# Kernel tuning notes

Measured on AMD Instinct MI355X. Metric: run time of the kernel, lower is better.

The kernel has to match this reference:

```python
import jax, jax.numpy as jnp
import numpy as np

N_NODES = 50000
N_EDGES = 262144
N_OCP = 32768
N_GRAPHS = 64
H = 128          # hidden_size
F_IN = 128       # node feature dim (== H for the stub GNN)
N_LABELS = 10


def _lin(key, fan_in, fan_out):
    return jax.random.normal(key, (fan_in, fan_out), jnp.float32) * (1.0 / float(np.sqrt(fan_in)))


def setup_inputs() -> dict:
    key = jax.random.key(0)
    ks = jax.random.split(key, 16)
    x = jax.random.normal(ks[0], (N_NODES, F_IN), jnp.float32)
    edge_index = jax.random.randint(ks[1], (2, N_EDGES), 0, N_NODES)
    batch_vec = jnp.sort(jax.random.randint(ks[2], (N_NODES,), 0, N_GRAPHS))
    y = jax.random.randint(ks[3], (N_GRAPHS,), 0, N_LABELS)
    params = {
        # stub GNN (get_node_reps): one GCN-style layer
        'W_self': _lin(ks[4], F_IN, H),
        'W_nbr': _lin(ks[5], F_IN, H),
        'b_gnn': jnp.zeros((H,), jnp.float32),
        # edge_action_rep_generator: Linear(2H,4H) ELU Linear(4H,2H) ELU Linear(2H,H)
        'Wr1': _lin(ks[6], 2 * H, 4 * H), 'br1': jnp.zeros((4 * H,), jnp.float32),
        'Wr2': _lin(ks[7], 4 * H, 2 * H), 'br2': jnp.zeros((2 * H,), jnp.float32),
        'Wr3': _lin(ks[8], 2 * H, H),     'br3': jnp.zeros((H,), jnp.float32),
        # edge_action_prob_generator: Linear(H,H) ELU Linear(H,num_labels)
        'Wp1': _lin(ks[9], H, H),         'bp1': jnp.zeros((H,), jnp.float32),
        'Wp2': _lin(ks[10], H, N_LABELS), 'bp2': jnp.zeros((N_LABELS,), jnp.float32),
    }
    return dict(x=x, edge_index=edge_index, batch_vec=batch_vec, y=y, n_ocp=N_OCP, **params)


def reference(x, edge_index, batch_vec, y, n_ocp,
              W_self, W_nbr, b_gnn,
              Wr1, br1, Wr2, br2, Wr3, br3,
              Wp1, bp1, Wp2, bp2):
    N = x.shape[0]
    G = y.shape[0]

    def get_node_reps(ei):
        # stub for self.model.get_node_reps: elu(x @ W_self + A @ (x @ W_nbr))
        msg = x[ei[0]] @ W_nbr                                   # [E', H]
        agg = jax.ops.segment_sum(msg, ei[1], num_segments=N)    # [N, H]
        return jax.nn.elu(x @ W_self + agg + b_gnn)

    ocp_edge_index = edge_index[:, :n_ocp]    # state == True edges
    ava_edge_index = edge_index[:, n_ocp:]    # state == False edges

    ava_node_reps = get_node_reps(edge_index) - get_node_reps(ocp_edge_index)  # [N, H]

    # gather per available edge + concat src/dst reps -> [E_ava, 2H]
    a = jnp.concatenate([ava_node_reps[ava_edge_index[0]],
                         ava_node_reps[ava_edge_index[1]]], axis=1)
    # edge_action_rep_generator
    a = jax.nn.elu(a @ Wr1 + br1)
    a = jax.nn.elu(a @ Wr2 + br2)
    a = a @ Wr3 + br3                                            # [E_ava, H]
    # edge_action_prob_generator
    h = jax.nn.elu(a @ Wp1 + bp1)
    logits = h @ Wp2 + bp2                                       # [E_ava, L]

    seg = batch_vec[ava_edge_index[0]]                           # graph id per ava edge
    y_edge = y[seg]                                              # target label per edge
    sel = jnp.take_along_axis(logits, y_edge[:, None], axis=1)[:, 0]  # gather(1, y)

    # segment-wise softmax over edges of each graph
    mx = jax.ops.segment_max(sel, seg, num_segments=G)
    ex = jnp.exp(sel - mx[seg])
    probs = ex / jax.ops.segment_sum(ex, seg, num_segments=G)[seg]    # [E_ava]

    # scatter_max: per-graph max prob and its argmax edge index
    pmax = jax.ops.segment_max(probs, seg, num_segments=G)            # [G]
    E = probs.shape[0]
    idx = jnp.where(probs == pmax[seg], jnp.arange(E), E)
    added_actions = jax.ops.segment_min(idx, seg, num_segments=G)     # [G]

    return probs, pmax, added_actions
```

## Files before the change

### kernel.cpp

```cpp
#include <hip/hip_runtime.h>

#define NN   50000
#define NNP  50048
#define NE   262144
#define NOCP 32768
#define EAVA (NE - NOCP)
#define NG   64
#define HD   128
#define CAP  48
#define CHNK 32768

typedef _Float16 f16x8 __attribute__((ext_vector_type(8)));
typedef _Float16 f16x2 __attribute__((ext_vector_type(2)));
typedef float f32x4 __attribute__((ext_vector_type(4)));

__device__ __forceinline__ float elu_f(float v) { return v > 0.f ? v : (expf(v) - 1.f); }

__device__ __forceinline__ unsigned fenc(float f) {
  unsigned u = __float_as_uint(f);
  return (u & 0x80000000u) ? ~u : (u | 0x80000000u);
}
__device__ __forceinline__ float fdec(unsigned u) {
  return __uint_as_float((u & 0x80000000u) ? (u & 0x7fffffffu) : ~u);
}

__device__ __forceinline__ void dma16(const void* g, void* l) {
  __builtin_amdgcn_global_load_lds((const __attribute__((address_space(1))) unsigned int*)g,
                                   (__attribute__((address_space(3))) unsigned int*)l,
                                   16, 0, 0);
}

__global__ __launch_bounds__(256) void zero_i(int* __restrict__ p, int n) {
  for (int i = blockIdx.x * 256 + threadIdx.x; i < n; i += gridDim.x * 256) p[i] = 0;
}

__global__ void init_small(unsigned* mx_enc, float* denom, unsigned* pmax_enc, int* amin) {
  int t = threadIdx.x;
  if (t < NG) { mx_enc[t] = 0u; denom[t] = 0.f; pmax_enc[t] = 0u; amin[t] = EAVA; }
}

__global__ __launch_bounds__(256) void zero_tails(_Float16* __restrict__ base) {
  int t = blockIdx.x * 256 + threadIdx.x;
  if (t >= 6 * 768) return;
  int arr = t / 768, off = t % 768;
  f16x8 z = {};
  *(f16x8*)(base + (size_t)arr * NNP * HD + (size_t)NN * HD + (size_t)off * 8) = z;
}

__global__ __launch_bounds__(256) void bucket_kernel(const int* __restrict__ ei,
    int* __restrict__ cnt, int* __restrict__ bucket) {
  int e = blockIdx.x * 256 + threadIdx.x;
  if (e >= NE) return;
  int dst = ei[NE + e];
  int slot = atomicAdd(&cnt[dst], 1);
  if (slot < CAP) bucket[(size_t)dst * CAP + slot] = e;
}

__global__ __launch_bounds__(256) void gather_kernel(const float* __restrict__ x,
    const int* __restrict__ ei, const int* __restrict__ cnt, const int* __restrict__ bucket,
    _Float16* __restrict__ xsah, _Float16* __restrict__ xsal,
    _Float16* __restrict__ xsoh, _Float16* __restrict__ xsol) {
  int n = blockIdx.x * 4 + (threadIdx.x >> 6);
  if (n >= NN) return;
  int lane = threadIdx.x & 63;
  int c = cnt[n];
  if (c > CAP) c = CAP;
  float2 aall = make_float2(0.f, 0.f), aocp = aall;
  const int* bk = bucket + (size_t)n * CAP;
  for (int i = 0; i < c; ++i) {
    int e = bk[i];
    int src = ei[e];
    float2 v = *(const float2*)(x + (size_t)src * HD + lane * 2);
    aall.x += v.x; aall.y += v.y;
    if (e < NOCP) { aocp.x += v.x; aocp.y += v.y; }
  }
  size_t o = (size_t)n * HD + lane * 2;
  _Float16 h0 = (_Float16)aall.x, h1 = (_Float16)aall.y;
  *(f16x2*)(xsah + o) = (f16x2){h0, h1};
  *(f16x2*)(xsal + o) = (f16x2){(_Float16)(aall.x - (float)h0), (_Float16)(aall.y - (float)h1)};
  _Float16 g0 = (_Float16)aocp.x, g1 = (_Float16)aocp.y;
  *(f16x2*)(xsoh + o) = (f16x2){g0, g1};
  *(f16x2*)(xsol + o) = (f16x2){(_Float16)(aocp.x - (float)g0), (_Float16)(aocp.y - (float)g1)};
}

__global__ __launch_bounds__(256) void split_x(const float* __restrict__ r,
    _Float16* __restrict__ rh, _Float16* __restrict__ rl) {
  int t = blockIdx.x * 256 + threadIdx.x;
  if (t >= NN * HD / 8) return;
  const float4* p = (const float4*)(r + (size_t)t * 8);
  float4 v0 = p[0], v1 = p[1];
  float vv[8] = {v0.x, v0.y, v0.z, v0.w, v1.x, v1.y, v1.z, v1.w};
  f16x8 hv, lv;
#pragma unroll
  for (int j = 0; j < 8; ++j) {
    _Float16 hh = (_Float16)vv[j];
    hv[j] = hh;
    lv[j] = (_Float16)(vv[j] - (float)hh);
  }
  *(f16x8*)(rh + (size_t)t * 8) = hv;
  *(f16x8*)(rl + (size_t)t * 8) = lv;
}

__global__ void pack_w2(const float* __restrict__ Wself, const float* __restrict__ Wnbr,
    _Float16* __restrict__ oh, _Float16* __restrict__ ol) {
  int chunk = blockIdx.x;
  int lane = threadIdx.x;
  int ns = chunk & 7, kt = chunk >> 3;
  int n = ns * 16 + (lane & 15);
  int k0 = kt * 32 + (lane >> 4) * 8;
  f16x8 hv, lv;
#pragma unroll
  for (int j = 0; j < 8; ++j) {
    int k = k0 + j;
    float v = (k < 128) ? Wself[(size_t)k * 128 + n] : Wnbr[(size_t)(k - 128) * 128 + n];
    _Float16 hh = (_Float16)v;
    hv[j] = hh;
    lv[j] = (_Float16)(v - (float)hh);
  }
  *(f16x8*)(oh + (size_t)chunk * 512 + lane * 8) = hv;
  *(f16x8*)(ol + (size_t)chunk * 512 + lane * 8) = lv;
}

__global__ void pack_w(const float* __restrict__ W, int K, int N,
    _Float16* __restrict__ oh, _Float16* __restrict__ ol) {
  int chunk = blockIdx.x;
  int lane = threadIdx.x;
  int NS = N >> 4;
  int ns = chunk % NS, kt = chunk / NS;
  int n = ns * 16 + (lane & 15);
  int k0 = kt * 32 + (lane >> 4) * 8;
  f16x8 hv, lv;
#pragma unroll
  for (int j = 0; j < 8; ++j) {
    float v = W[(size_t)(k0 + j) * N + n];
    _Float16 hh = (_Float16)v;
    hv[j] = hh;
    lv[j] = (_Float16)(v - (float)hh);
  }
  *(f16x8*)(oh + (size_t)chunk * 512 + lane * 8) = hv;
  *(f16x8*)(ol + (size_t)chunk * 512 + lane * 8) = lv;
}

__global__ void w34_kernel(const float* __restrict__ Wr3, const float* __restrict__ Wp1,
    const float* __restrict__ br3, const float* __restrict__ bp1,
    float* __restrict__ W34, float* __restrict__ b34) {
  int i = blockIdx.x, j = threadIdx.x;
  float s = 0.f;
  for (int k = 0; k < 128; ++k) s += Wr3[i * 128 + k] * Wp1[k * 128 + j];
  W34[i * 128 + j] = s;
  if (i == 0) {
    float t = bp1[j];
    for (int k = 0; k < 128; ++k) t += br3[k] * Wp1[k * 128 + j];
    b34[j] = t;
  }
}

template <int KT, int NS_B, int AMODE, int KT_NEXT>
__global__ __launch_bounds__(256) void gemm_ab(
    const _Float16* __restrict__ Ah, const _Float16* __restrict__ Al,
    const int* __restrict__ idx0, const int* __restrict__ idx1,
    const _Float16* __restrict__ Bh, const _Float16* __restrict__ Bl,
    const float* __restrict__ bias,
    _Float16* __restrict__ Oh, _Float16* __restrict__ Ol) {
  __shared__ char smem[65536] __attribute__((aligned(16)));
  float* sC = (float*)smem;

  const int tid = threadIdx.x;
  const int w = tid >> 6, lane = tid & 63;
  const int l16 = lane & 15, g16 = lane >> 4;
  const int bm = blockIdx.x * 128, bn = blockIdx.y * 128;
  const int mw = (w >> 1) * 4, nw = (w & 1) * 4;
  const int bmT = bm >> 4, bnS = bn >> 4;

  f32x4 acc[4][4];
#pragma unroll
  for (int i = 0; i < 4; ++i)
#pragma unroll
    for (int j = 0; j < 4; ++j) acc[i][j] = (f32x4)0.f;

  int i0a = 0, i0b = 0, i1a = 0, i1b = 0;
  if constexpr (AMODE == 1) {
    int rr0 = bm + w * 32 + l16;
    i0a = idx0[rr0]; i0b = idx0[rr0 + 16];
    i1a = idx1[rr0]; i1b = idx1[rr0 + 16];
  }

  auto STAGE = [&](int kt, int buf) {
    char* base = smem + buf * 32768;
    if constexpr (AMODE == 0) {
#pragma unroll
      for (int s = 0; s < 2; ++s) {
        int msub = w * 2 + s;
        size_t ch = (size_t)(bmT + msub) * KT + kt;
        dma16((const char*)Ah + ch * 1024 + lane * 16, base + msub * 1024);
        dma16((const char*)Al + ch * 1024 + lane * 16, base + 8192 + msub * 1024);
      }
    } else {
      int col = (kt & 3) * 32 + g16 * 8;
      int r0 = (kt < 4) ? i0a : i1a;
      int r1 = (kt < 4) ? i0b : i1b;
      dma16(Ah + (size_t)r0 * HD + col, base + (w * 2) * 1024);
      dma16(Al + (size_t)r0 * HD + col, base + 8192 + (w * 2) * 1024);
      dma16(Ah + (size_t)r1 * HD + col, base + (w * 2 + 1) * 1024);
      dma16(Al + (size_t)r1 * HD + col, base + 8192 + (w * 2 + 1) * 1024);
    }
#pragma unroll
    for (int s = 0; s < 2; ++s) {
      int nsub = w * 2 + s;
      size_t ch = (size_t)kt * NS_B + bnS + nsub;
      dma16((const char*)Bh + ch * 1024 + lane * 16, base + 16384 + nsub * 1024);
      dma16((const char*)Bl + ch * 1024 + lane * 16, base + 24576 + nsub * 1024);
    }
  };

  auto COMPUTE = [&](int buf) {
    const _Float16* sAh = (const _Float16*)(smem + buf * 32768);
    const _Float16* sAl = (const _Float16*)(smem + buf * 32768 + 8192);
    const _Float16* sBh = (const _Float16*)(smem + buf * 32768 + 16384);
    const _Float16* sBl = (const _Float16*)(smem + buf * 32768 + 24576);
    f16x8 ah[4], al[4];
#pragma unroll
    for (int mi = 0; mi < 4; ++mi) {
      ah[mi] = *(const f16x8*)(sAh + (mw + mi) * 512 + lane * 8);
      al[mi] = *(const f16x8*)(sAl + (mw + mi) * 512 + lane * 8);
    }
#pragma unroll
    for (int ni = 0; ni < 4; ++ni) {
      f16x8 bh = *(const f16x8*)(sBh + (nw + ni) * 512 + lane * 8);
      f16x8 bl = *(const f16x8*)(sBl + (nw + ni) * 512 + lane * 8);
#pragma unroll
      for (int mi = 0; mi < 4; ++mi) {
        acc[mi][ni] = __builtin_amdgcn_mfma_f32_16x16x32_f16(ah[mi], bh, acc[mi][ni], 0, 0, 0);
        acc[mi][ni] = __builtin_amdgcn_mfma_f32_16x16x32_f16(al[mi], bh, acc[mi][ni], 0, 0, 0);
        acc[mi][ni] = __builtin_amdgcn_mfma_f32_16x16x32_f16(ah[mi], bl, acc[mi][ni], 0, 0, 0);
      }
    }
  };

  STAGE(0, 0);
  __builtin_amdgcn_s_waitcnt(0);
  __syncthreads();
  for (int kt = 0; kt < KT; kt += 2) {
    STAGE(kt + 1, 1);
    COMPUTE(0);
    __builtin_amdgcn_s_waitcnt(0);
    __syncthreads();
    if (kt + 2 < KT) STAGE(kt + 2, 0);
    COMPUTE(1);
    __builtin_amdgcn_s_waitcnt(0);
    __syncthreads();
  }

  const int bnT32 = bn >> 5;
  for (int ph = 0; ph < 2; ++ph) {
    if ((w & 1) == ph) {
#pragma unroll
      for (int ni = 0; ni < 4; ++ni) {
        int colL = ni * 16 + l16;
        float bv = bias[bn + ph * 64 + colL];
#pragma unroll
        for (int mi = 0; mi < 4; ++mi) {
          int rowb = (mw + mi) * 16 + g16 * 4;
#pragma unroll
          for (int r = 0; r < 4; ++r)
            sC[(rowb + r) * 68 + colL] = elu_f(acc[mi][ni][r] + bv);
        }
      }
    }
    __syncthreads();
#pragma unroll
    for (int c = 0; c < 4; ++c) {
      int chunkid = w * 4 + c;
      int msub = chunkid >> 1, ktl = chunkid & 1;
      int m = msub * 16 + l16;
      int cb = ktl * 32 + g16 * 8;
      f16x8 hv, lv;
#pragma unroll
      for (int j = 0; j < 8; ++j) {
        float v = sC[m * 68 + cb + j];
        _Float16 hh = (_Float16)v;
        hv[j] = hh;
        lv[j] = (_Float16)(v - (float)hh);
      }
      size_t gchunk = (size_t)(bmT + msub) * KT_NEXT + (bnT32 + ph * 2 + ktl);
      *(f16x8*)((char*)Oh + gchunk * 1024 + lane * 16) = hv;
      *(f16x8*)((char*)Ol + gchunk * 1024 + lane * 16) = lv;
    }
    __syncthreads();
  }
}

__global__ __launch_bounds__(64) void reps_direct(
    const _Float16* __restrict__ xh, const _Float16* __restrict__ xl,
    const _Float16* __restrict__ xsah, const _Float16* __restrict__ xsal,
    const _Float16* __restrict__ xsoh, const _Float16* __restrict__ xsol,
    const _Float16* __restrict__ Wsh, const _Float16* __restrict__ Wsl,
    const float* __restrict__ bias,
    _Float16* __restrict__ Oh, _Float16* __restrict__ Ol) {
  __shared__ float sC[64][68];
  const int lane = threadIdx.x;
  const int mt = blockIdx.x, nt = blockIdx.y;
  const int bm = mt * 64, bn = nt * 64;
  const int l16 = lane & 15, g16 = lane >> 4;

  f32x4 acc1[4][4], acc2[4][4];
#pragma unroll
  for (int i = 0; i < 4; ++i)
#pragma unroll
    for (int j = 0; j < 4; ++j) acc1[i][j] = (f32x4)0.f;

  auto CP3 = [&](f32x4 (*acc)[4], const f16x8* ah, const f16x8* al,
                 const f16x8* bh, const f16x8* bl) {
#pragma unroll
    for (int ni = 0; ni < 4; ++ni)
#pragma unroll
      for (int mi = 0; mi < 4; ++mi) {
        acc[mi][ni] = __builtin_amdgcn_mfma_f32_16x16x32_f16(ah[mi], bh[ni], acc[mi][ni], 0, 0, 0);
        acc[mi][ni] = __builtin_amdgcn_mfma_f32_16x16x32_f16(al[mi], bh[ni], acc[mi][ni], 0, 0, 0);
        acc[mi][ni] = __builtin_amdgcn_mfma_f32_16x16x32_f16(ah[mi], bl[ni], acc[mi][ni], 0, 0, 0);
      }
  };

#pragma unroll
  for (int kt = 0; kt < 4; ++kt) {
    f16x8 ah[4], al[4], bh[4], bl[4];
#pragma unroll
    for (int mi = 0; mi < 4; ++mi) {
      size_t off = (size_t)(bm + mi * 16 + l16) * HD + kt * 32 + g16 * 8;
      ah[mi] = *(const f16x8*)(xh + off);
      al[mi] = *(const f16x8*)(xl + off);
    }
#pragma unroll
    for (int ni = 0; ni < 4; ++ni) {
      size_t ch = (size_t)kt * 8 + nt * 4 + ni;
      bh[ni] = *(const f16x8*)(Wsh + ch * 512 + lane * 8);
      bl[ni] = *(const f16x8*)(Wsl + ch * 512 + lane * 8);
    }
    CP3(acc1, ah, al, bh, bl);
  }
#pragma unroll
  for (int i = 0; i < 4; ++i)
#pragma unroll
    for (int j = 0; j < 4; ++j) acc2[i][j] = acc1[i][j];

#pragma unroll
  for (int kt = 0; kt < 4; ++kt) {
    f16x8 aah[4], aal[4], aoh[4], aol[4], bh[4], bl[4];
#pragma unroll
    for (int mi = 0; mi < 4; ++mi) {
      size_t off = (size_t)(bm + mi * 16 + l16) * HD + kt * 32 + g16 * 8;
      aah[mi] = *(const f16x8*)(xsah + off);
      aal[mi] = *(const f16x8*)(xsal + off);
      aoh[mi] = *(const f16x8*)(xsoh + off);
      aol[mi] = *(const f16x8*)(xsol + off);
    }
#pragma unroll
    for (int ni = 0; ni < 4; ++ni) {
      size_t ch = (size_t)(kt + 4) * 8 + nt * 4 + ni;
      bh[ni] = *(const f16x8*)(Wsh + ch * 512 + lane * 8);
      bl[ni] = *(const f16x8*)(Wsl + ch * 512 + lane * 8);
    }
    CP3(acc1, aah, aal, bh, bl);
    CP3(acc2, aoh, aol, bh, bl);
  }

#pragma unroll
  for (int ni = 0; ni < 4; ++ni) {
    int colL = ni * 16 + l16;
    float bv = bias[bn + colL];
#pragma unroll
    for (int mi = 0; mi < 4; ++mi) {
      int rowb = mi * 16 + g16 * 4;
#pragma unroll
      for (int r = 0; r < 4; ++r)
        sC[rowb + r][colL] = elu_f(acc1[mi][ni][r] + bv) - elu_f(acc2[mi][ni][r] + bv);
    }
  }
  __syncthreads();
#pragma unroll
  for (int c = 0; c < 8; ++c) {
    int msub = c >> 1, ktl = c & 1;
    int m = msub * 16 + l16;
    int cb = ktl * 32 + g16 * 8;
    int grow = bm + m;
    if (grow < NN) {
      f16x8 hv, lv;
#pragma unroll
      for (int j = 0; j < 8; ++j) {
        float v = sC[m][cb + j];
        _Float16 hh = (_Float16)v;
        hv[j] = hh;
        lv[j] = (_Float16)(v - (float)hh);
      }
      *(f16x8*)(Oh + (size_t)grow * HD + bn + cb) = hv;
      *(f16x8*)(Ol + (size_t)grow * HD + bn + cb) = lv;
    }
  }
}

__global__ __launch_bounds__(256) void gemm3_sel(
    const _Float16* __restrict__ Ah, const _Float16* __restrict__ Al,
    const _Float16* __restrict__ Bh, const _Float16* __restrict__ Bl,
    const float* __restrict__ b34,
    const int* __restrict__ ei, const int* __restrict__ batchv, const int* __restrict__ yv,
    const float* __restrict__ Wp2, const float* __restrict__ bp2,
    float* __restrict__ sel, int* __restrict__ seg, int co) {
  __shared__ char smem[65536] __attribute__((aligned(16)));
  const int tid = threadIdx.x;
  const int w = tid >> 6, lane = tid & 63;
  const int l16 = lane & 15, g16 = lane >> 4;
  const int mt = blockIdx.x;

  f32x4 acc[2][8];
#pragma unroll
  for (int i = 0; i < 2; ++i)
#pragma unroll
    for (int j = 0; j < 8; ++j) acc[i][j] = (f32x4)0.f;

  auto STAGE = [&](int kt, int buf) {
    char* base = smem + buf * 32768;
#pragma unroll
    for (int s = 0; s < 2; ++s) {
      int msub = w * 2 + s;
      size_t ch = (size_t)(mt * 8 + msub) * 8 + kt;
      dma16((const char*)Ah + ch * 1024 + lane * 16, base + msub * 1024);
      dma16((const char*)Al + ch * 1024 + lane * 16, base + 8192 + msub * 1024);
    }
#pragma unroll
    for (int s = 0; s < 2; ++s) {
      int nsub = w * 2 + s;
      size_t ch = (size_t)kt * 8 + nsub;
      dma16((const char*)Bh + ch * 1024 + lane * 16, base + 16384 + nsub * 1024);
      dma16((const char*)Bl + ch * 1024 + lane * 16, base + 24576 + nsub * 1024);
    }
  };

  auto COMPUTE = [&](int buf) {
    const _Float16* sAh = (const _Float16*)(smem + buf * 32768);
    const _Float16* sAl = (const _Float16*)(smem + buf * 32768 + 8192);
    const _Float16* sBh = (const _Float16*)(smem + buf * 32768 + 16384);
    const _Float16* sBl = (const _Float16*)(smem + buf * 32768 + 24576);
    f16x8 ah[2], al[2];
#pragma unroll
    for (int mi = 0; mi < 2; ++mi) {
      ah[mi] = *(const f16x8*)(sAh + (w * 2 + mi) * 512 + lane * 8);
      al[mi] = *(const f16x8*)(sAl + (w * 2 + mi) * 512 + lane * 8);
    }
#pragma unroll
    for (int ni = 0; ni < 8; ++ni) {
      f16x8 bh = *(const f16x8*)(sBh + ni * 512 + lane * 8);
      f16x8 bl = *(const f16x8*)(sBl + ni * 512 + lane * 8);
#pragma unroll
      for (int mi = 0; mi < 2; ++mi) {
        acc[mi][ni] = __builtin_amdgcn_mfma_f32_16x16x32_f16(ah[mi], bh, acc[mi][ni], 0, 0, 0);
        acc[mi][ni] = __builtin_amdgcn_mfma_f32_16x16x32_f16(al[mi], bh, acc[mi][ni], 0, 0, 0);
        acc[mi][ni] = __builtin_amdgcn_mfma_f32_16x16x32_f16(ah[mi], bl, acc[mi][ni], 0, 0, 0);
      }
    }
  };

  STAGE(0, 0);
  __builtin_amdgcn_s_waitcnt(0);
  __syncthreads();
  for (int kt = 0; kt < 8; kt += 2) {
    STAGE(kt + 1, 1);
    COMPUTE(0);
    __builtin_amdgcn_s_waitcnt(0);
    __syncthreads();
    if (kt + 2 < 8) STAGE(kt + 2, 0);
    COMPUTE(1);
    __builtin_amdgcn_s_waitcnt(0);
    __syncthreads();
  }

  float bb[8];
#pragma unroll
  for (int ni = 0; ni < 8; ++ni) bb[ni] = b34[ni * 16 + l16];

#pragma unroll
  for (int mi = 0; mi < 2; ++mi)
#pragma unroll
    for (int rr = 0; rr < 4; ++rr) {
      int row = w * 32 + mi * 16 + g16 * 4 + rr;
      int e = co + mt * 128 + row;
      int s = ei[NOCP + e];
      int gg = batchv[s];
      int c = yv[gg];
      float a = 0.f;
#pragma unroll
      for (int ni = 0; ni < 8; ++ni)
        a += elu_f(acc[mi][ni][rr] + bb[ni]) * Wp2[(ni * 16 + l16) * 10 + c];
      a += __shfl_xor(a, 1);
      a += __shfl_xor(a, 2);
      a += __shfl_xor(a, 4);
      a += __shfl_xor(a, 8);
      if (l16 == 0) { sel[e] = a + bp2[c]; seg[e] = gg; }
    }
}

__global__ __launch_bounds__(256) void segmax_sel(const float* __restrict__ sel,
    const int* __restrict__ seg, unsigned* __restrict__ mx_enc) {
  __shared__ unsigned sm[NG];
  int tid = threadIdx.x;
  if (tid < NG) sm[tid] = 0u;
  __syncthreads();
  for (int i = blockIdx.x * blockDim.x + tid; i < EAVA; i += gridDim.x * blockDim.x)
    atomicMax(&sm[seg[i]], fenc(sel[i]));
  __syncthreads();
  if (tid < NG) atomicMax(&mx_enc[tid], sm[tid]);
}

__global__ __launch_bounds__(256) void exden_kernel(const float* __restrict__ sel,
    const int* __restrict__ seg, const unsigned* __restrict__ mx_enc,
    float* __restrict__ denom, float* __restrict__ out_probs) {
  __shared__ float sd[NG];
  __shared__ float smx[NG];
  int tid = threadIdx.x;
  if (tid < NG) { smx[tid] = fdec(mx_enc[tid]); sd[tid] = 0.f; }
  __syncthreads();
  for (int i = blockIdx.x * blockDim.x + tid; i < EAVA; i += gridDim.x * blockDim.x) {
    int g = seg[i];
    float ex = expf(sel[i] - smx[g]);
    out_probs[i] = ex;
    atomicAdd(&sd[g], ex);
  }
  __syncthreads();
  if (tid < NG) atomicAdd(&denom[tid], sd[tid]);
}

__global__ __launch_bounds__(256) void probpmax_kernel(const int* __restrict__ seg,
    const float* __restrict__ denom, float* __restrict__ out_probs,
    unsigned* __restrict__ pmax_enc) {
  __shared__ float sden[NG];
  __shared__ unsigned sp[NG];
  int tid = threadIdx.x;
  if (tid < NG) { sden[tid] = denom[tid]; sp[tid] = 0u; }
  __syncthreads();
  for (int i = blockIdx.x * blockDim.x + tid; i < EAVA; i += gridDim.x * blockDim.x) {
    int g = seg[i];
    float p = out_probs[i] / sden[g];
    out_probs[i] = p;
    atomicMax(&sp[g], fenc(p));
  }
  __syncthreads();
  if (tid < NG) atomicMax(&pmax_enc[tid], sp[tid]);
}

__global__ __launch_bounds__(256) void argmin_kernel(const int* __restrict__ seg,
    const float* __restrict__ out_probs, const unsigned* __restrict__ pmax_enc,
    int* __restrict__ amin) {
  __shared__ float spm[NG];
  __shared__ int sa[NG];
  int tid = threadIdx.x;
  if (tid < NG) { spm[tid] = fdec(pmax_enc[tid]); sa[tid] = EAVA; }
  __syncthreads();
  for (int i = blockIdx.x * blockDim.x + tid; i < EAVA; i += gridDim.x * blockDim.x) {
    int g = seg[i];
    if (out_probs[i] == spm[g]) atomicMin(&sa[g], i);
  }
  __syncthreads();
  if (tid < NG) atomicMin(&amin[tid], sa[tid]);
}

__global__ void finalize_kernel(const unsigned* __restrict__ pmax_enc,
    const int* __restrict__ amin, float* __restrict__ out) {
  int g = threadIdx.x;
  if (g < NG) {
    out[EAVA + g] = fdec(pmax_enc[g]);
    out[EAVA + NG + g] = (float)amin[g];
  }
}

extern "C" void kernel_launch(void* const* d_in, const int* in_sizes, int n_in,
                              void* d_out, int out_size, void* d_ws, size_t ws_size,
                              hipStream_t stream) {
  const float* x      = (const float*)d_in[0];
  const int*   ei     = (const int*)d_in[1];
  const int*   batchv = (const int*)d_in[2];
  const int*   yv     = (const int*)d_in[3];
  const float* Wself = (const float*)d_in[5];
  const float* Wnbr  = (const float*)d_in[6];
  const float* bgnn  = (const float*)d_in[7];
  const float* Wr1   = (const float*)d_in[8];
  const float* br1   = (const float*)d_in[9];
  const float* Wr2   = (const float*)d_in[10];
  const float* br2   = (const float*)d_in[11];
  const float* Wr3   = (const float*)d_in[12];
  const float* br3   = (const float*)d_in[13];
  const float* Wp1   = (const float*)d_in[14];
  const float* bp1   = (const float*)d_in[15];
  const float* Wp2   = (const float*)d_in[16];
  const float* bp2   = (const float*)d_in[17];
  float* out = (float*)d_out;

  char* wp = (char*)d_ws;
  auto alloc = [&](size_t bytes) -> char* {
    char* p = wp;
    wp += (bytes + 255) & ~(size_t)255;
    return p;
  };
  _Float16* xsplit = (_Float16*)alloc((size_t)6 * NNP * HD * 2);
  _Float16* xh   = xsplit + (size_t)0 * NNP * HD;
  _Float16* xl   = xsplit + (size_t)1 * NNP * HD;
  _Float16* xsah = xsplit + (size_t)2 * NNP * HD;
  _Float16* xsal = xsplit + (size_t)3 * NNP * HD;
  _Float16* xsoh = xsplit + (size_t)4 * NNP * HD;
  _Float16* xsol = xsplit + (size_t)5 * NNP * HD;
  _Float16*  reps_h   = (_Float16*)alloc((size_t)NN * HD * 2);
  _Float16*  reps_l   = (_Float16*)alloc((size_t)NN * HD * 2);
  int*       cnt      = (int*)alloc((size_t)NN * 4);
  int*       bucket   = (int*)alloc((size_t)NN * CAP * 4);
  float*     sel      = (float*)alloc((size_t)EAVA * 4);
  int*       seg      = (int*)alloc((size_t)EAVA * 4);
  unsigned*  mx_enc   = (unsigned*)alloc(NG * 4);
  float*     denom    = (float*)alloc(NG * 4);
  unsigned*  pmax_enc = (unsigned*)alloc(NG * 4);
  int*       amin     = (int*)alloc(NG * 4);
  _Float16*  Wsh  = (_Float16*)alloc((size_t)64 * 1024);
  _Float16*  Wsl  = (_Float16*)alloc((size_t)64 * 1024);
  _Float16*  Wr1h = (_Float16*)alloc((size_t)8 * 32 * 1024);
  _Float16*  Wr1l = (_Float16*)alloc((size_t)8 * 32 * 1024);
  _Float16*  Wr2h = (_Float16*)alloc((size_t)16 * 16 * 1024);
  _Float16*  Wr2l = (_Float16*)alloc((size_t)16 * 16 * 1024);
  float*     W34  = (float*)alloc((size_t)256 * 128 * 4);
  float*     b34  = (float*)alloc(128 * 4);
  _Float16*  W34h = (_Float16*)alloc((size_t)8 * 8 * 1024);
  _Float16*  W34l = (_Float16*)alloc((size_t)8 * 8 * 1024);
  _Float16*  b1h = (_Float16*)alloc((size_t)(CHNK / 16) * 16 * 1024);
  _Float16*  b1l = (_Float16*)alloc((size_t)(CHNK / 16) * 16 * 1024);
  _Float16*  b2h = (_Float16*)alloc((size_t)(CHNK / 16) * 8 * 1024);
  _Float16*  b2l = (_Float16*)alloc((size_t)(CHNK / 16) * 8 * 1024);
  (void)ws_size;

  zero_i<<<64, 256, 0, stream>>>(cnt, NN);
  init_small<<<1, 64, 0, stream>>>(mx_enc, denom, pmax_enc, amin);
  zero_tails<<<18, 256, 0, stream>>>(xsplit);
  bucket_kernel<<<NE / 256, 256, 0, stream>>>(ei, cnt, bucket);
  gather_kernel<<<(NN + 3) / 4, 256, 0, stream>>>(x, ei, cnt, bucket, xsah, xsal, xsoh, xsol);
  split_x<<<(NN * HD / 8 + 255) / 256, 256, 0, stream>>>(x, xh, xl);
  pack_w2<<<64, 64, 0, stream>>>(Wself, Wnbr, Wsh, Wsl);
  reps_direct<<<dim3(NNP / 64, 2), 64, 0, stream>>>(xh, xl, xsah, xsal, xsoh, xsol, Wsh, Wsl,
                                                    bgnn, reps_h, reps_l);
  w34_kernel<<<256, 128, 0, stream>>>(Wr3, Wp1, br3, bp1, W34, b34);
  pack_w<<<8 * 32, 64, 0, stream>>>(Wr1, 256, 512, Wr1h, Wr1l);
  pack_w<<<16 * 16, 64, 0, stream>>>(Wr2, 512, 256, Wr2h, Wr2l);
  pack_w<<<8 * 8, 64, 0, stream>>>(W34, 256, 128, W34h, W34l);

  for (int c = 0; c < 7; ++c) {
    int co = c * CHNK;
    gemm_ab<8, 32, 1, 16><<<dim3(CHNK / 128, 4), 256, 0, stream>>>(
        reps_h, reps_l, ei + NOCP + co, ei + NE + NOCP + co, Wr1h, Wr1l, br1, b1h, b1l);
    gemm_ab<16, 16, 0, 8><<<dim3(CHNK / 128, 2), 256, 0, stream>>>(
        b1h, b1l, nullptr, nullptr, Wr2h, Wr2l, br2, b2h, b2l);
    gemm3_sel<<<CHNK / 128, 256, 0, stream>>>(
        b2h, b2l, W34h, W34l, b34, ei, batchv, yv, Wp2, bp2, sel, seg, co);
  }

  segmax_sel<<<112, 256, 0, stream>>>(sel, seg, mx_enc);
  exden_kernel<<<112, 256, 0, stream>>>(sel, seg, mx_enc, denom, out);
  probpmax_kernel<<<112, 256, 0, stream>>>(seg, denom, out, pmax_enc);
  argmin_kernel<<<112, 256, 0, stream>>>(seg, out, pmax_enc, amin);
  finalize_kernel<<<1, 64, 0, stream>>>(pmax_enc, amin, out);
}
```

Measured before the change: 990.3 us.

## Fuse second MLP GEMM into final GEMM and pack src/ocp flag into buckets

The second edge-MLP GEMM (512->256 with ELU) is merged into the final selection kernel. Each 64-column slice of its output is computed, passed through ELU and staged in shared memory, split into fp16 hi/lo, and immediately multiplied against W34, so the b2 intermediate is never written to or read from global memory. This also removes one launch per chunk, but each block now handles all 256 columns, so the grid is half as wide and W34 fragments are read straight from global memory. Separately, the bucket kernel stores the source node index with the OCP flag in the sign bit, and the gather kernel reads four bucket entries at once, removing the dependent load through edge_index and exposing more memory-level parallelism.

```diff
diff --git a/kernel.cpp b/kernel.cpp
--- a/kernel.cpp
+++ b/kernel.cpp
@@ -52,12 +52,14 @@
   int e = blockIdx.x * 256 + threadIdx.x;
   if (e >= NE) return;
   int dst = ei[NE + e];
+  int src = ei[e];
   int slot = atomicAdd(&cnt[dst], 1);
-  if (slot < CAP) bucket[(size_t)dst * CAP + slot] = e;
+  if (slot < CAP)
+    bucket[(size_t)dst * CAP + slot] = (int)((unsigned)src | (e < NOCP ? 0x80000000u : 0u));
 }
 
 __global__ __launch_bounds__(256) void gather_kernel(const float* __restrict__ x,
-    const int* __restrict__ ei, const int* __restrict__ cnt, const int* __restrict__ bucket,
+    const int* __restrict__ cnt, const int* __restrict__ bucket,
     _Float16* __restrict__ xsah, _Float16* __restrict__ xsal,
     _Float16* __restrict__ xsoh, _Float16* __restrict__ xsol) {
   int n = blockIdx.x * 4 + (threadIdx.x >> 6);
@@ -67,12 +69,22 @@
   if (c > CAP) c = CAP;
   float2 aall = make_float2(0.f, 0.f), aocp = aall;
   const int* bk = bucket + (size_t)n * CAP;
-  for (int i = 0; i < c; ++i) {
-    int e = bk[i];
-    int src = ei[e];
-    float2 v = *(const float2*)(x + (size_t)src * HD + lane * 2);
-    aall.x += v.x; aall.y += v.y;
-    if (e < NOCP) { aocp.x += v.x; aocp.y += v.y; }
+  for (int i0 = 0; i0 < c; i0 += 4) {
+    int4 pk = *(const int4*)(bk + i0);
+    bool m1 = (i0 + 1 < c), m2 = (i0 + 2 < c), m3 = (i0 + 3 < c);
+    int r0 = pk.x & 0x7fffffff;
+    int r1 = m1 ? (pk.y & 0x7fffffff) : 0;
+    int r2 = m2 ? (pk.z & 0x7fffffff) : 0;
+    int r3 = m3 ? (pk.w & 0x7fffffff) : 0;
+    float2 v0 = *(const float2*)(x + (size_t)r0 * HD + lane * 2);
+    float2 v1 = *(const float2*)(x + (size_t)r1 * HD + lane * 2);
+    float2 v2 = *(const float2*)(x + (size_t)r2 * HD + lane * 2);
+    float2 v3 = *(const float2*)(x + (size_t)r3 * HD + lane * 2);
+    aall.x += v0.x; aall.y += v0.y;
+    if (pk.x < 0) { aocp.x += v0.x; aocp.y += v0.y; }
+    if (m1) { aall.x += v1.x; aall.y += v1.y; if (pk.y < 0) { aocp.x += v1.x; aocp.y += v1.y; } }
+    if (m2) { aall.x += v2.x; aall.y += v2.y; if (pk.z < 0) { aocp.x += v2.x; aocp.y += v2.y; } }
+    if (m3) { aall.x += v3.x; aall.y += v3.y; if (pk.w < 0) { aocp.x += v3.x; aocp.y += v3.y; } }
   }
   size_t o = (size_t)n * HD + lane * 2;
   _Float16 h0 = (_Float16)aall.x, h1 = (_Float16)aall.y;
@@ -398,78 +410,130 @@
   }
 }
 
-__global__ __launch_bounds__(256) void gemm3_sel(
+__global__ __launch_bounds__(256) void gemm23_sel(
     const _Float16* __restrict__ Ah, const _Float16* __restrict__ Al,
     const _Float16* __restrict__ Bh, const _Float16* __restrict__ Bl,
+    const float* __restrict__ br2,
+    const _Float16* __restrict__ W34h, const _Float16* __restrict__ W34l,
     const float* __restrict__ b34,
     const int* __restrict__ ei, const int* __restrict__ batchv, const int* __restrict__ yv,
     const float* __restrict__ Wp2, const float* __restrict__ bp2,
     float* __restrict__ sel, int* __restrict__ seg, int co) {
-  __shared__ char smem[65536] __attribute__((aligned(16)));
+  __shared__ char smem[49152] __attribute__((aligned(16)));
+  float* sC = (float*)smem;
   const int tid = threadIdx.x;
   const int w = tid >> 6, lane = tid & 63;
   const int l16 = lane & 15, g16 = lane >> 4;
   const int mt = blockIdx.x;
 
-  f32x4 acc[2][8];
+  f32x4 lacc[2][8];
 #pragma unroll
   for (int i = 0; i < 2; ++i)
 #pragma unroll
-    for (int j = 0; j < 8; ++j) acc[i][j] = (f32x4)0.f;
-
-  auto STAGE = [&](int kt, int buf) {
-    char* base = smem + buf * 32768;
-#pragma unroll
-    for (int s = 0; s < 2; ++s) {
-      int msub = w * 2 + s;
-      size_t ch = (size_t)(mt * 8 + msub) * 8 + kt;
-      dma16((const char*)Ah + ch * 1024 + lane * 16, base + msub * 1024);
-      dma16((const char*)Al + ch * 1024 + lane * 16, base + 8192 + msub * 1024);
-    }
-#pragma unroll
-    for (int s = 0; s < 2; ++s) {
-      int nsub = w * 2 + s;
-      size_t ch = (size_t)kt * 8 + nsub;
-      dma16((const char*)Bh + ch * 1024 + lane * 16, base + 16384 + nsub * 1024);
-      dma16((const char*)Bl + ch * 1024 + lane * 16, base + 24576 + nsub * 1024);
-    }
-  };
-
-  auto COMPUTE = [&](int buf) {
-    const _Float16* sAh = (const _Float16*)(smem + buf * 32768);
-    const _Float16* sAl = (const _Float16*)(smem + buf * 32768 + 8192);
-    const _Float16* sBh = (const _Float16*)(smem + buf * 32768 + 16384);
-    const _Float16* sBl = (const _Float16*)(smem + buf * 32768 + 24576);
-    f16x8 ah[2], al[2];
-#pragma unroll
-    for (int mi = 0; mi < 2; ++mi) {
-      ah[mi] = *(const f16x8*)(sAh + (w * 2 + mi) * 512 + lane * 8);
-      al[mi] = *(const f16x8*)(sAl + (w * 2 + mi) * 512 + lane * 8);
-    }
-#pragma unroll
-    for (int ni = 0; ni < 8; ++ni) {
-      f16x8 bh = *(const f16x8*)(sBh + ni * 512 + lane * 8);
-      f16x8 bl = *(const f16x8*)(sBl + ni * 512 + lane * 8);
+    for (int j = 0; j < 8; ++j) lacc[i][j] = (f32x4)0.f;
+
+  for (int ks = 0; ks < 4; ++ks) {
+    f32x4 sacc[2][4];
+#pragma unroll
+    for (int i = 0; i < 2; ++i)
+#pragma unroll
+      for (int j = 0; j < 4; ++j) sacc[i][j] = (f32x4)0.f;
+
+    auto STAGE = [&](int kt, int buf) {
+      char* base = smem + buf * 24576;
+#pragma unroll
+      for (int s = 0; s < 2; ++s) {
+        int msub = w * 2 + s;
+        size_t ch = (size_t)(mt * 8 + msub) * 16 + kt;
+        dma16((const char*)Ah + ch * 1024 + lane * 16, base + msub * 1024);
+        dma16((const char*)Al + ch * 1024 + lane * 16, base + 8192 + msub * 1024);
+      }
+      size_t chb = (size_t)kt * 16 + ks * 4 + w;
+      dma16((const char*)Bh + chb * 1024 + lane * 16, base + 16384 + w * 1024);
+      dma16((const char*)Bl + chb * 1024 + lane * 16, base + 20480 + w * 1024);
+    };
+
+    auto COMPUTE = [&](int buf) {
+      const _Float16* sAh = (const _Float16*)(smem + buf * 24576);
+      const _Float16* sAl = (const _Float16*)(smem + buf * 24576 + 8192);
+      const _Float16* sBh = (const _Float16*)(smem + buf * 24576 + 16384);
+      const _Float16* sBl = (const _Float16*)(smem + buf * 24576 + 20480);
+      f16x8 ah[2], al[2];
 #pragma unroll
       for (int mi = 0; mi < 2; ++mi) {
-        acc[mi][ni] = __builtin_amdgcn_mfma_f32_16x16x32_f16(ah[mi], bh, acc[mi][ni], 0, 0, 0);
-        acc[mi][ni] = __builtin_amdgcn_mfma_f32_16x16x32_f16(al[mi], bh, acc[mi][ni], 0, 0, 0);
-        acc[mi][ni] = __builtin_amdgcn_mfma_f32_16x16x32_f16(ah[mi], bl, acc[mi][ni], 0, 0, 0);
-      }
-    }
-  };
-
-  STAGE(0, 0);
-  __builtin_amdgcn_s_waitcnt(0);
-  __syncthreads();
-  for (int kt = 0; kt < 8; kt += 2) {
-    STAGE(kt + 1, 1);
-    COMPUTE(0);
+        ah[mi] = *(const f16x8*)(sAh + (w * 2 + mi) * 512 + lane * 8);
+        al[mi] = *(const f16x8*)(sAl + (w * 2 + mi) * 512 + lane * 8);
+      }
+#pragma unroll
+      for (int ni = 0; ni < 4; ++ni) {
+        f16x8 bh = *(const f16x8*)(sBh + ni * 512 + lane * 8);
+        f16x8 bl = *(const f16x8*)(sBl + ni * 512 + lane * 8);
+#pragma unroll
+        for (int mi = 0; mi < 2; ++mi) {
+          sacc[mi][ni] = __builtin_amdgcn_mfma_f32_16x16x32_f16(ah[mi], bh, sacc[mi][ni], 0, 0, 0);
+          sacc[mi][ni] = __builtin_amdgcn_mfma_f32_16x16x32_f16(al[mi], bh, sacc[mi][ni], 0, 0, 0);
+          sacc[mi][ni] = __builtin_amdgcn_mfma_f32_16x16x32_f16(ah[mi], bl, sacc[mi][ni], 0, 0, 0);
+        }
+      }
+    };
+
+    STAGE(0, 0);
     __builtin_amdgcn_s_waitcnt(0);
     __syncthreads();
-    if (kt + 2 < 8) STAGE(kt + 2, 0);
-    COMPUTE(1);
-    __builtin_amdgcn_s_waitcnt(0);
+    for (int kt = 0; kt < 16; kt += 2) {
+      STAGE(kt + 1, 1);
+      COMPUTE(0);
+      __builtin_amdgcn_s_waitcnt(0);
+      __syncthreads();
+      if (kt + 2 < 16) STAGE(kt + 2, 0);
+      COMPUTE(1);
+      __builtin_amdgcn_s_waitcnt(0);
+      __syncthreads();
+    }
+
+#pragma unroll
+    for (int ni = 0; ni < 4; ++ni) {
+      int colL = ni * 16 + l16;
+      float bv = br2[ks * 64 + colL];
+#pragma unroll
+      for (int mi = 0; mi < 2; ++mi) {
+        int rowb = w * 32 + mi * 16 + g16 * 4;
+#pragma unroll
+        for (int r = 0; r < 4; ++r)
+          sC[(rowb + r) * 68 + colL] = elu_f(sacc[mi][ni][r] + bv);
+      }
+    }
+    __syncthreads();
+
+#pragma unroll
+    for (int kk = 0; kk < 2; ++kk) {
+      int kt3 = ks * 2 + kk;
+      f16x8 pah[2], pal[2];
+#pragma unroll
+      for (int mi = 0; mi < 2; ++mi) {
+        int row = w * 32 + mi * 16 + l16;
+        const float* src = sC + (size_t)row * 68 + kk * 32 + g16 * 8;
+#pragma unroll
+        for (int j = 0; j < 8; ++j) {
+          float v = src[j];
+          _Float16 hh = (_Float16)v;
+          pah[mi][j] = hh;
+          pal[mi][j] = (_Float16)(v - (float)hh);
+        }
+      }
+#pragma unroll
+      for (int ni = 0; ni < 8; ++ni) {
+        size_t ch = (size_t)kt3 * 8 + ni;
+        f16x8 bh = *(const f16x8*)(W34h + ch * 512 + lane * 8);
+        f16x8 bl = *(const f16x8*)(W34l + ch * 512 + lane * 8);
+#pragma unroll
+        for (int mi = 0; mi < 2; ++mi) {
+          lacc[mi][ni] = __builtin_amdgcn_mfma_f32_16x16x32_f16(pah[mi], bh, lacc[mi][ni], 0, 0, 0);
+          lacc[mi][ni] = __builtin_amdgcn_mfma_f32_16x16x32_f16(pal[mi], bh, lacc[mi][ni], 0, 0, 0);
+          lacc[mi][ni] = __builtin_amdgcn_mfma_f32_16x16x32_f16(pah[mi], bl, lacc[mi][ni], 0, 0, 0);
+        }
+      }
+    }
     __syncthreads();
   }
 
@@ -489,7 +553,7 @@
       float a = 0.f;
 #pragma unroll
       for (int ni = 0; ni < 8; ++ni)
-        a += elu_f(acc[mi][ni][rr] + bb[ni]) * Wp2[(ni * 16 + l16) * 10 + c];
+        a += elu_f(lacc[mi][ni][rr] + bb[ni]) * Wp2[(ni * 16 + l16) * 10 + c];
       a += __shfl_xor(a, 1);
       a += __shfl_xor(a, 2);
       a += __shfl_xor(a, 4);
@@ -628,15 +692,13 @@
   _Float16*  W34l = (_Float16*)alloc((size_t)8 * 8 * 1024);
   _Float16*  b1h = (_Float16*)alloc((size_t)(CHNK / 16) * 16 * 1024);
   _Float16*  b1l = (_Float16*)alloc((size_t)(CHNK / 16) * 16 * 1024);
-  _Float16*  b2h = (_Float16*)alloc((size_t)(CHNK / 16) * 8 * 1024);
-  _Float16*  b2l = (_Float16*)alloc((size_t)(CHNK / 16) * 8 * 1024);
   (void)ws_size;
 
   zero_i<<<64, 256, 0, stream>>>(cnt, NN);
   init_small<<<1, 64, 0, stream>>>(mx_enc, denom, pmax_enc, amin);
   zero_tails<<<18, 256, 0, stream>>>(xsplit);
   bucket_kernel<<<NE / 256, 256, 0, stream>>>(ei, cnt, bucket);
-  gather_kernel<<<(NN + 3) / 4, 256, 0, stream>>>(x, ei, cnt, bucket, xsah, xsal, xsoh, xsol);
+  gather_kernel<<<(NN + 3) / 4, 256, 0, stream>>>(x, cnt, bucket, xsah, xsal, xsoh, xsol);
   split_x<<<(NN * HD / 8 + 255) / 256, 256, 0, stream>>>(x, xh, xl);
   pack_w2<<<64, 64, 0, stream>>>(Wself, Wnbr, Wsh, Wsl);
   reps_direct<<<dim3(NNP / 64, 2), 64, 0, stream>>>(xh, xl, xsah, xsal, xsoh, xsol, Wsh, Wsl,
@@ -650,10 +712,9 @@
     int co = c * CHNK;
     gemm_ab<8, 32, 1, 16><<<dim3(CHNK / 128, 4), 256, 0, stream>>>(
         reps_h, reps_l, ei + NOCP + co, ei + NE + NOCP + co, Wr1h, Wr1l, br1, b1h, b1l);
-    gemm_ab<16, 16, 0, 8><<<dim3(CHNK / 128, 2), 256, 0, stream>>>(
-        b1h, b1l, nullptr, nullptr, Wr2h, Wr2l, br2, b2h, b2l);
-    gemm3_sel<<<CHNK / 128, 256, 0, stream>>>(
-        b2h, b2l, W34h, W34l, b34, ei, batchv, yv, Wp2, bp2, sel, seg, co);
+    gemm23_sel<<<CHNK / 128, 256, 0, stream>>>(
+        b1h, b1l, Wr2h, Wr2l, br2, W34h, W34l, b34,
+        ei, batchv, yv, Wp2, bp2, sel, seg, co);
   }
 
   segmax_sel<<<112, 256, 0, stream>>>(sel, seg, mx_enc);
```

Result: slower. 1.173 ms (+18.4%).

## Pack source id and ocp flag into buckets; halve gemm3_sel row tile

Applied to the files above, without the earlier changes.

The bucket kernel now stores the source node with the occupied-edge flag in the sign bit, so the gather no longer does a dependent load of ei per edge. The gather loop also loads four bucket entries at once and issues four independent row loads per iteration to raise memory-level parallelism. gemm3_sel is retiled from 128 to 64 rows per block, which doubles the grid (512 blocks per chunk), cuts LDS use and accumulator registers, and targets higher occupancy. The cost is that B tiles are reloaded twice as often per row.

```diff
diff --git a/kernel.cpp b/kernel.cpp
--- a/kernel.cpp
+++ b/kernel.cpp
@@ -52,12 +52,14 @@
   int e = blockIdx.x * 256 + threadIdx.x;
   if (e >= NE) return;
   int dst = ei[NE + e];
+  int src = ei[e];
   int slot = atomicAdd(&cnt[dst], 1);
-  if (slot < CAP) bucket[(size_t)dst * CAP + slot] = e;
+  if (slot < CAP)
+    bucket[(size_t)dst * CAP + slot] = (int)((unsigned)src | (e < NOCP ? 0x80000000u : 0u));
 }
 
 __global__ __launch_bounds__(256) void gather_kernel(const float* __restrict__ x,
-    const int* __restrict__ ei, const int* __restrict__ cnt, const int* __restrict__ bucket,
+    const int* __restrict__ cnt, const int* __restrict__ bucket,
     _Float16* __restrict__ xsah, _Float16* __restrict__ xsal,
     _Float16* __restrict__ xsoh, _Float16* __restrict__ xsol) {
   int n = blockIdx.x * 4 + (threadIdx.x >> 6);
@@ -67,12 +69,22 @@
   if (c > CAP) c = CAP;
   float2 aall = make_float2(0.f, 0.f), aocp = aall;
   const int* bk = bucket + (size_t)n * CAP;
-  for (int i = 0; i < c; ++i) {
-    int e = bk[i];
-    int src = ei[e];
-    float2 v = *(const float2*)(x + (size_t)src * HD + lane * 2);
-    aall.x += v.x; aall.y += v.y;
-    if (e < NOCP) { aocp.x += v.x; aocp.y += v.y; }
+  for (int i0 = 0; i0 < c; i0 += 4) {
+    int4 pk = *(const int4*)(bk + i0);
+    bool m1 = (i0 + 1 < c), m2 = (i0 + 2 < c), m3 = (i0 + 3 < c);
+    int r0 = pk.x & 0x7fffffff;
+    int r1 = m1 ? (pk.y & 0x7fffffff) : 0;
+    int r2 = m2 ? (pk.z & 0x7fffffff) : 0;
+    int r3 = m3 ? (pk.w & 0x7fffffff) : 0;
+    float2 v0 = *(const float2*)(x + (size_t)r0 * HD + lane * 2);
+    float2 v1 = *(const float2*)(x + (size_t)r1 * HD + lane * 2);
+    float2 v2 = *(const float2*)(x + (size_t)r2 * HD + lane * 2);
+    float2 v3 = *(const float2*)(x + (size_t)r3 * HD + lane * 2);
+    aall.x += v0.x; aall.y += v0.y;
+    if (pk.x < 0) { aocp.x += v0.x; aocp.y += v0.y; }
+    if (m1) { aall.x += v1.x; aall.y += v1.y; if (pk.y < 0) { aocp.x += v1.x; aocp.y += v1.y; } }
+    if (m2) { aall.x += v2.x; aall.y += v2.y; if (pk.z < 0) { aocp.x += v2.x; aocp.y += v2.y; } }
+    if (m3) { aall.x += v3.x; aall.y += v3.y; if (pk.w < 0) { aocp.x += v3.x; aocp.y += v3.y; } }
   }
   size_t o = (size_t)n * HD + lane * 2;
   _Float16 h0 = (_Float16)aall.x, h1 = (_Float16)aall.y;
@@ -405,57 +417,44 @@
     const int* __restrict__ ei, const int* __restrict__ batchv, const int* __restrict__ yv,
     const float* __restrict__ Wp2, const float* __restrict__ bp2,
     float* __restrict__ sel, int* __restrict__ seg, int co) {
-  __shared__ char smem[65536] __attribute__((aligned(16)));
+  __shared__ char smem[49152] __attribute__((aligned(16)));
   const int tid = threadIdx.x;
   const int w = tid >> 6, lane = tid & 63;
   const int l16 = lane & 15, g16 = lane >> 4;
   const int mt = blockIdx.x;
 
-  f32x4 acc[2][8];
-#pragma unroll
-  for (int i = 0; i < 2; ++i)
-#pragma unroll
-    for (int j = 0; j < 8; ++j) acc[i][j] = (f32x4)0.f;
+  f32x4 acc[8];
+#pragma unroll
+  for (int j = 0; j < 8; ++j) acc[j] = (f32x4)0.f;
 
   auto STAGE = [&](int kt, int buf) {
-    char* base = smem + buf * 32768;
-#pragma unroll
-    for (int s = 0; s < 2; ++s) {
-      int msub = w * 2 + s;
-      size_t ch = (size_t)(mt * 8 + msub) * 8 + kt;
-      dma16((const char*)Ah + ch * 1024 + lane * 16, base + msub * 1024);
-      dma16((const char*)Al + ch * 1024 + lane * 16, base + 8192 + msub * 1024);
-    }
+    char* base = smem + buf * 24576;
+    size_t ch = (size_t)(mt * 4 + w) * 8 + kt;
+    dma16((const char*)Ah + ch * 1024 + lane * 16, base + w * 1024);
+    dma16((const char*)Al + ch * 1024 + lane * 16, base + 4096 + w * 1024);
 #pragma unroll
     for (int s = 0; s < 2; ++s) {
       int nsub = w * 2 + s;
-      size_t ch = (size_t)kt * 8 + nsub;
-      dma16((const char*)Bh + ch * 1024 + lane * 16, base + 16384 + nsub * 1024);
-      dma16((const char*)Bl + ch * 1024 + lane * 16, base + 24576 + nsub * 1024);
+      size_t chb = (size_t)kt * 8 + nsub;
+      dma16((const char*)Bh + chb * 1024 + lane * 16, base + 8192 + nsub * 1024);
+      dma16((const char*)Bl + chb * 1024 + lane * 16, base + 16384 + nsub * 1024);
     }
   };
 
   auto COMPUTE = [&](int buf) {
-    const _Float16* sAh = (const _Float16*)(smem + buf * 32768);
-    const _Float16* sAl = (const _Float16*)(smem + buf * 32768 + 8192);
-    const _Float16* sBh = (const _Float16*)(smem + buf * 32768 + 16384);
-    const _Float16* sBl = (const _Float16*)(smem + buf * 32768 + 24576);
-    f16x8 ah[2], al[2];
-#pragma unroll
-    for (int mi = 0; mi < 2; ++mi) {
-      ah[mi] = *(const f16x8*)(sAh + (w * 2 + mi) * 512 + lane * 8);
-      al[mi] = *(const f16x8*)(sAl + (w * 2 + mi) * 512 + lane * 8);
-    }
+    const _Float16* sAh = (const _Float16*)(smem + buf * 24576);
+    const _Float16* sAl = (const _Float16*)(smem + buf * 24576 + 4096);
+    const _Float16* sBh = (const _Float16*)(smem + buf * 24576 + 8192);
+    const _Float16* sBl = (const _Float16*)(smem + buf * 24576 + 16384);
+    f16x8 ah = *(const f16x8*)(sAh + w * 512 + lane * 8);
+    f16x8 al = *(const f16x8*)(sAl + w * 512 + lane * 8);
 #pragma unroll
     for (int ni = 0; ni < 8; ++ni) {
       f16x8 bh = *(const f16x8*)(sBh + ni * 512 + lane * 8);
       f16x8 bl = *(const f16x8*)(sBl + ni * 512 + lane * 8);
-#pragma unroll
-      for (int mi = 0; mi < 2; ++mi) {
-        acc[mi][ni] = __builtin_amdgcn_mfma_f32_16x16x32_f16(ah[mi], bh, acc[mi][ni], 0, 0, 0);
-        acc[mi][ni] = __builtin_amdgcn_mfma_f32_16x16x32_f16(al[mi], bh, acc[mi][ni], 0, 0, 0);
-        acc[mi][ni] = __builtin_amdgcn_mfma_f32_16x16x32_f16(ah[mi], bl, acc[mi][ni], 0, 0, 0);
-      }
+      acc[ni] = __builtin_amdgcn_mfma_f32_16x16x32_f16(ah, bh, acc[ni], 0, 0, 0);
+      acc[ni] = __builtin_amdgcn_mfma_f32_16x16x32_f16(al, bh, acc[ni], 0, 0, 0);
+      acc[ni] = __builtin_amdgcn_mfma_f32_16x16x32_f16(ah, bl, acc[ni], 0, 0, 0);
     }
   };
 
@@ -478,24 +477,22 @@
   for (int ni = 0; ni < 8; ++ni) bb[ni] = b34[ni * 16 + l16];
 
 #pragma unroll
-  for (int mi = 0; mi < 2; ++mi)
-#pragma unroll
-    for (int rr = 0; rr < 4; ++rr) {
-      int row = w * 32 + mi * 16 + g16 * 4 + rr;
-      int e = co + mt * 128 + row;
-      int s = ei[NOCP + e];
-      int gg = batchv[s];
-      int c = yv[gg];
-      float a = 0.f;
-#pragma unroll
-      for (int ni = 0; ni < 8; ++ni)
-        a += elu_f(acc[mi][ni][rr] + bb[ni]) * Wp2[(ni * 16 + l16) * 10 + c];
-      a += __shfl_xor(a, 1);
-      a += __shfl_xor(a, 2);
-      a += __shfl_xor(a, 4);
-      a += __shfl_xor(a, 8);
-      if (l16 == 0) { sel[e] = a + bp2[c]; seg[e] = gg; }
-    }
+  for (int rr = 0; rr < 4; ++rr) {
+    int row = w * 16 + g16 * 4 + rr;
+    int e = co + mt * 64 + row;
+    int s = ei[NOCP + e];
+    int gg = batchv[s];
+    int c = yv[gg];
+    float a = 0.f;
+#pragma unroll
+    for (int ni = 0; ni < 8; ++ni)
+      a += elu_f(acc[ni][rr] + bb[ni]) * Wp2[(ni * 16 + l16) * 10 + c];
+    a += __shfl_xor(a, 1);
+    a += __shfl_xor(a, 2);
+    a += __shfl_xor(a, 4);
+    a += __shfl_xor(a, 8);
+    if (l16 == 0) { sel[e] = a + bp2[c]; seg[e] = gg; }
+  }
 }
 
 __global__ __launch_bounds__(256) void segmax_sel(const float* __restrict__ sel,
@@ -636,7 +633,7 @@
   init_small<<<1, 64, 0, stream>>>(mx_enc, denom, pmax_enc, amin);
   zero_tails<<<18, 256, 0, stream>>>(xsplit);
   bucket_kernel<<<NE / 256, 256, 0, stream>>>(ei, cnt, bucket);
-  gather_kernel<<<(NN + 3) / 4, 256, 0, stream>>>(x, ei, cnt, bucket, xsah, xsal, xsoh, xsol);
+  gather_kernel<<<(NN + 3) / 4, 256, 0, stream>>>(x, cnt, bucket, xsah, xsal, xsoh, xsol);
   split_x<<<(NN * HD / 8 + 255) / 256, 256, 0, stream>>>(x, xh, xl);
   pack_w2<<<64, 64, 0, stream>>>(Wself, Wnbr, Wsh, Wsl);
   reps_direct<<<dim3(NNP / 64, 2), 64, 0, stream>>>(xh, xl, xsah, xsal, xsoh, xsol, Wsh, Wsl,
@@ -652,7 +649,7 @@
         reps_h, reps_l, ei + NOCP + co, ei + NE + NOCP + co, Wr1h, Wr1l, br1, b1h, b1l);
     gemm_ab<16, 16, 0, 8><<<dim3(CHNK / 128, 2), 256, 0, stream>>>(
         b1h, b1l, nullptr, nullptr, Wr2h, Wr2l, br2, b2h, b2l);
-    gemm3_sel<<<CHNK / 128, 256, 0, stream>>>(
+    gemm3_sel<<<CHNK / 64, 256, 0, stream>>>(
         b2h, b2l, W34h, W34l, b34, ei, batchv, yv, Wp2, bp2, sel, seg, co);
   }
 
```

New measurement: 971.1 us. No clear change (-1.9%).
